# Kernel tuning notes

Hardware: AMD Instinct MI355X
Metric: run time of the kernel (lower is better)

## Reference

```python
import jax, jax.numpy as jnp
import numpy as np

HID = 256      # hard-coded hidden_size in the torch module
LEVELS = 16    # topological levels in the generated DAG


def _lstm_cell(x, h, c, Wih, Whh, bih, bhh):
    # PyTorch LSTM cell: gates ordered (input, forget, cell, output)
    g = x @ Wih.T + h @ Whh.T + bih + bhh
    i, f, gg, o = jnp.split(g, 4, axis=-1)
    c_new = jax.nn.sigmoid(f) * c + jax.nn.sigmoid(i) * jnp.tanh(gg)
    h_new = jax.nn.sigmoid(o) * jnp.tanh(c_new)
    return h_new, c_new


def _forward(tokens, parents_idx, parent_valid,
             Wih_tok, Whh_tok, bih_tok, bhh_tok,
             Wih_ins, Whh_ins, bih_ins, bhh_ins, Wlin, blin):
    N, T, E = tokens.shape
    K = N // LEVELS
    NEG = jnp.asarray(-1e30, tokens.dtype)

    # --- token-level LSTM over each instruction's tokens, batched across instrs ---
    def tok_step(carry, x):
        h, c = carry
        return _lstm_cell(x, h, c, Wih_tok, Whh_tok, bih_tok, bhh_tok), None
    z = jnp.zeros((N, HID), tokens.dtype)
    (ins_embed, _), _ = jax.lax.scan(tok_step, (z, z), tokens.transpose(1, 0, 2))
    # ins_embed: [N, HID] = final token-LSTM hidden per instruction

    # --- instruction-level LSTM over the DAG, level by level ---
    H = jnp.zeros((N, HID), tokens.dtype)
    C = jnp.zeros((N, HID), tokens.dtype)
    for l in range(LEVELS):
        sl = slice(l * K, (l + 1) * K)
        pidx = parents_idx[sl]                 # [K, P] indices into earlier levels
        pval = parent_valid[sl][..., None]     # [K, P, 1]
        ph = jnp.where(pval, H[pidx], NEG).max(axis=1)   # max-reduction combine
        pc = jnp.where(pval, C[pidx], NEG).max(axis=1)
        has = parent_valid[sl].any(axis=1, keepdims=True)
        h0 = jnp.where(has, ph, 0.0)           # no parents -> zero init_hidden
        c0 = jnp.where(has, pc, 0.0)
        h1, c1 = _lstm_cell(ins_embed[sl], h0, c0, Wih_ins, Whh_ins, bih_ins, bhh_ins)
        H = H.at[sl].set(h1)
        C = C.at[sl].set(c1)

    # roots = instructions with no children (never referenced as a parent)
    appears = jnp.zeros((N,), jnp.int32).at[parents_idx.reshape(-1)].add(
        parent_valid.reshape(-1).astype(jnp.int32))
    root = (appears == 0)[:, None]
    final = jnp.where(root, H, NEG).max(axis=0)   # [HID]
    return final @ Wlin.T + blin                   # [num_classes]


def setup_inputs() -> dict:
    N, T, E, P = 2048, 16, 512, 8
    K = N // LEVELS
    rng = np.random.default_rng(0)
    pidx = np.zeros((N, P), np.int32)
    pval = np.zeros((N, P), bool)
    for l in range(1, LEVELS):
        pidx[l * K:(l + 1) * K] = rng.integers(0, l * K, (K, P))
        pval[l * K:(l + 1) * K] = rng.random((K, P)) < 0.75
    key = jax.random.key(0)
    ks = jax.random.split(key, 6)
    s = lambda k, shape, fan: jax.random.normal(k, shape, jnp.float32) / np.float32(np.sqrt(fan))
    return {
        "tokens": jax.random.normal(ks[0], (N, T, E), jnp.float32),
        "parents_idx": jnp.asarray(pidx),
        "parent_valid": jnp.asarray(pval),
        "Wih_tok": s(ks[1], (4 * HID, E), E),
        "Whh_tok": s(ks[2], (4 * HID, HID), HID),
        "bih_tok": jnp.zeros((4 * HID,), jnp.float32),
        "bhh_tok": jnp.zeros((4 * HID,), jnp.float32),
        "Wih_ins": s(ks[3], (4 * HID, HID), HID),
        "Whh_ins": s(ks[4], (4 * HID, HID), HID),
        "bih_ins": jnp.zeros((4 * HID,), jnp.float32),
        "bhh_ins": jnp.zeros((4 * HID,), jnp.float32),
        "Wlin": s(ks[5], (1, HID), HID),
        "blin": jnp.zeros((1,), jnp.float32),
    }


def reference(tokens, parents_idx, parent_valid,
              Wih_tok, Whh_tok, bih_tok, bhh_tok,
              Wih_ins, Whh_ins, bih_ins, bhh_ins, Wlin, blin):
    return _forward(tokens, parents_idx, parent_valid,
                    Wih_tok, Whh_tok, bih_tok, bhh_tok,
                    Wih_ins, Whh_ins, bih_ins, bhh_ins, Wlin, blin)
```

## Files before the change

kernel.cpp:

```cpp
#include <hip/hip_runtime.h>

#define NTOK 2048
#define TT   16
#define EE   512
#define HIDD 256
#define G4   1024
#define NLVL 16
#define KLVL 128
#define INV2048 (1.0f/2048.0f)

typedef _Float16 v8h __attribute__((ext_vector_type(8)));
typedef _Float16 v4h __attribute__((ext_vector_type(4)));
typedef float    v4f __attribute__((ext_vector_type(4)));

__device__ __forceinline__ v4f mfma16(v8h a, v8h b, v4f c) {
  return __builtin_amdgcn_mfma_f32_16x16x32_f16(a, b, c, 0, 0, 0);
}

__device__ __forceinline__ float fsig(float x) {
  return 1.0f / (1.0f + __expf(-x));
}
__device__ __forceinline__ float ftanh(float x) {
  float ax = fabsf(x);
  float e  = __expf(-2.0f * ax);
  float t  = (1.0f - e) / (1.0f + e);
  return copysignf(t, x);
}

__device__ __forceinline__ void split8(const v4f& w0, const v4f& w1, v8h& hi, v8h& lo) {
#pragma unroll
  for (int u = 0; u < 4; ++u) {
    float v = w0[u]; _Float16 h = (_Float16)v;
    hi[u] = h; lo[u] = (_Float16)((v - (float)h) * 2048.0f);
  }
#pragma unroll
  for (int u = 0; u < 4; ++u) {
    float v = w1[u]; _Float16 h = (_Float16)v;
    hi[4+u] = h; lo[4+u] = (_Float16)((v - (float)h) * 2048.0f);
  }
}

__device__ __forceinline__ v8h cvt8(const v4f& w0, const v4f& w1) {
  v8h r;
#pragma unroll
  for (int u = 0; u < 4; ++u) { r[u] = (_Float16)w0[u]; r[4+u] = (_Float16)w1[u]; }
  return r;
}

__global__ __launch_bounds__(256) void knorm(const void* __restrict__ pv_raw,
                                             unsigned char* __restrict__ pv8) {
  __shared__ int mode;
  const int tid = threadIdx.x;
  if (tid == 0) mode = 0;
  __syncthreads();
  const unsigned* pu = (const unsigned*)pv_raw;
  int local = 0;
  for (int i = tid; i < 4096; i += 256) {
    unsigned v = pu[i];
    if (v == 0x3F800000u) { local = 2; break; }
    if (v > 1u) local = 1;
  }
  if (local) atomicMax(&mode, local);
  __syncthreads();
  const int m = mode;
  const unsigned char* pb = (const unsigned char*)pv_raw;
  const float* pf = (const float*)pv_raw;
  const int* pi = (const int*)pv_raw;
  for (int i = tid; i < NTOK * 8; i += 256) {
    unsigned char v;
    if (m == 1)      v = (pb[i] != 0);
    else if (m == 2) v = (pf[i] != 0.0f);
    else             v = (pi[i] != 0);
    pv8[i] = v;
  }
}

__global__ __launch_bounds__(256) void kw_cvt(
    const float* __restrict__ a0, _Float16* __restrict__ f0,
    const float* __restrict__ a1, _Float16* __restrict__ f1,
    const float* __restrict__ a2, _Float16* __restrict__ f2,
    const float* __restrict__ a3, _Float16* __restrict__ f3) {
  const int t = blockIdx.x * 256 + threadIdx.x;
  if (t < 32768) {
    const int row = t >> 5, col8 = (t & 31) * 8;
    const int fc = row >> 4, l15 = row & 15;
    const int kk = col8 >> 5, lq = (col8 >> 3) & 3;
    const int lane8 = (lq * 16 + l15) * 8;
    const size_t srow = (size_t)row * 256 + col8;
    {
      v4f x0 = *(const v4f*)(a0 + srow), x1 = *(const v4f*)(a0 + srow + 4);
      *(v8h*)(f0 + (size_t)(fc * 8 + kk) * 512 + lane8) = cvt8(x0, x1);
    }
    {
      v4f x0 = *(const v4f*)(a1 + srow), x1 = *(const v4f*)(a1 + srow + 4);
      v8h hi, lo; split8(x0, x1, hi, lo);
      _Float16* d = f1 + (size_t)(fc * 8 + kk) * 1024 + lane8;
      *(v8h*)d = hi; *(v8h*)(d + 512) = lo;
    }
    {
      v4f x0 = *(const v4f*)(a2 + srow), x1 = *(const v4f*)(a2 + srow + 4);
      v8h hi, lo; split8(x0, x1, hi, lo);
      _Float16* d = f2 + (size_t)(fc * 8 + kk) * 1024 + lane8;
      *(v8h*)d = hi; *(v8h*)(d + 512) = lo;
    }
  } else {
    const int k = t - 32768;
    const int row = k >> 6, col8 = (k & 63) * 8;
    const int fc = row >> 4, l15 = row & 15;
    const int kk = col8 >> 5, lq = (col8 >> 3) & 3;
    const size_t srow = (size_t)row * 512 + col8;
    v4f x0 = *(const v4f*)(a3 + srow), x1 = *(const v4f*)(a3 + srow + 4);
    *(v8h*)(f3 + (size_t)(fc * 16 + kk) * 512 + (lq * 16 + l15) * 8) = cvt8(x0, x1);
  }
}

__global__ __launch_bounds__(512, 1) void kg2(const float* __restrict__ A,
                                              const _Float16* __restrict__ WtH,
                                              const float* __restrict__ b1,
                                              const float* __restrict__ b2,
                                              _Float16* __restrict__ Xg, int h) {
  __shared__ _Float16 As[64 * 520];
  const int tid  = threadIdx.x;
  const int lane = tid & 63;
  const int nq   = tid >> 6;
  const int l15  = lane & 15;
  const int lq   = lane >> 4;
  const int m0   = blockIdx.x * 64;

#pragma unroll
  for (int p = 0; p < 4; ++p) {
    const int row  = p * 16 + (tid >> 5);
    const int col0 = (tid & 31) * 16;
    const int ar   = m0 + row;
    const int tokrow = (ar & 2047) * 16 + h * 8 + (ar >> 11);
    const float* s = A + (size_t)tokrow * EE + col0;
    v4f x0 = *(const v4f*)s, x1 = *(const v4f*)(s + 4);
    v4f x2 = *(const v4f*)(s + 8), x3 = *(const v4f*)(s + 12);
    _Float16* d = As + row * 520 + col0;
    *(v8h*)d       = cvt8(x0, x1);
    *(v8h*)(d + 8) = cvt8(x2, x3);
  }
  __syncthreads();

  v4f acc[4][8];
#pragma unroll
  for (int n = 0; n < 8; ++n) {
    const int col = (nq * 8 + n) * 16 + l15;
    const float bb = b1[col] + b2[col];
#pragma unroll
    for (int m = 0; m < 4; ++m) acc[m][n] = (v4f){bb, bb, bb, bb};
  }

#pragma unroll 4
  for (int kk = 0; kk < 16; ++kk) {
    v8h af[4];
#pragma unroll
    for (int m = 0; m < 4; ++m)
      af[m] = *(const v8h*)(As + (m * 16 + l15) * 520 + kk * 32 + lq * 8);
#pragma unroll
    for (int n = 0; n < 8; ++n) {
      const int fc = nq * 8 + n;
      v8h bh = *(const v8h*)(WtH + (size_t)(fc * 16 + kk) * 512 + lane * 8);
#pragma unroll
      for (int m = 0; m < 4; ++m) acc[m][n] = mfma16(af[m], bh, acc[m][n]);
    }
  }

#pragma unroll
  for (int m = 0; m < 4; ++m)
#pragma unroll
    for (int n = 0; n < 8; ++n) {
      const int row = m0 + m * 16 + lq * 4;
      const int col = (nq * 8 + n) * 16 + l15;
      v4h o;
#pragma unroll
      for (int r = 0; r < 4; ++r) o[r] = (_Float16)acc[m][n][r];
      *(v4h*)(Xg + ((size_t)(row >> 2) * G4 + col) * 4) = o;
    }
}

__global__ __launch_bounds__(512, 1) void kr3(const _Float16* __restrict__ Xg,
                                              const _Float16* __restrict__ WhhH,
                                              float* __restrict__ Hst,
                                              float* __restrict__ Cst,
                                              _Float16* __restrict__ emb, int q) {
  __shared__ float hbuf[2][16 * 260];
  const int tid  = threadIdx.x;
  const int lane = tid & 63;
  const int w    = tid >> 6;
  const int wv   = w & 3;
  const int jh   = w >> 2;
  const int l15  = lane & 15;
  const int lq   = lane >> 4;
  const int r0   = blockIdx.x * 16;

  const _Float16* wbase = WhhH + (size_t)(8 * jh + wv) * 4096 + lane * 8;

  v4f c[2];
  if (q) {
#pragma unroll
    for (int j2 = 0; j2 < 2; ++j2) {
      const int feat = 16 * (wv + 4 * (2 * jh + j2)) + l15;
#pragma unroll
      for (int r = 0; r < 4; ++r)
        c[j2][r] = Cst[(size_t)(r0 + lq * 4 + r) * HIDD + feat];
    }
    for (int idx = tid; idx < 4096; idx += 512)
      hbuf[0][(idx >> 8) * 260 + (idx & 255)] = Hst[(size_t)(r0 + (idx >> 8)) * HIDD + (idx & 255)];
  } else {
    c[0] = (v4f){0.f, 0.f, 0.f, 0.f};
    c[1] = (v4f){0.f, 0.f, 0.f, 0.f};
  }

  v4h xp[4][2];
  {
    const size_t xrow = (size_t)((r0 >> 2) + lq) * G4;
#pragma unroll
    for (int g = 0; g < 4; ++g)
#pragma unroll
      for (int j2 = 0; j2 < 2; ++j2) {
        const int col = 256 * g + 16 * (wv + 4 * (2 * jh + j2)) + l15;
        xp[g][j2] = *(const v4h*)(Xg + (xrow + col) * 4);
      }
  }

  v8h bA[8], bB[8];
#pragma unroll
  for (int g = 0; g < 4; ++g)
#pragma unroll
    for (int j2 = 0; j2 < 2; ++j2)
      bA[g * 2 + j2] = *(const v8h*)(wbase + (16 * g + 4 * j2) * 4096);
  __syncthreads();

#pragma unroll 1
  for (int tl = 0; tl < 8; ++tl) {
    const int cur = tl & 1;
    const bool have_h = (q > 0) || (tl > 0);
    v4f acc[4][2];
#pragma unroll
    for (int g = 0; g < 4; ++g)
#pragma unroll
      for (int j2 = 0; j2 < 2; ++j2) {
        v4f a;
#pragma unroll
        for (int r = 0; r < 4; ++r) a[r] = (float)xp[g][j2][r];
        acc[g][j2] = a;
      }
    if (tl < 7) {
      const size_t xrow = (size_t)((tl + 1) * 512 + (r0 >> 2) + lq) * G4;
#pragma unroll
      for (int g = 0; g < 4; ++g)
#pragma unroll
        for (int j2 = 0; j2 < 2; ++j2) {
          const int col = 256 * g + 16 * (wv + 4 * (2 * jh + j2)) + l15;
          xp[g][j2] = *(const v4h*)(Xg + (xrow + col) * 4);
        }
    }
    if (have_h) {
#pragma unroll
      for (int kp = 0; kp < 4; ++kp) {
        const int k0 = 2 * kp, k1 = 2 * kp + 1;
#pragma unroll
        for (int g = 0; g < 4; ++g)
#pragma unroll
          for (int j2 = 0; j2 < 2; ++j2)
            bB[g * 2 + j2] = *(const v8h*)(wbase + (16 * g + 4 * j2) * 4096 + k1 * 512);
        {
          const int ko = k0 * 32 + lq * 8;
          v4f w0 = *(const v4f*)(hbuf[cur] + l15 * 260 + ko);
          v4f w1 = *(const v4f*)(hbuf[cur] + l15 * 260 + ko + 4);
          v8h ah = cvt8(w0, w1);
#pragma unroll
          for (int g = 0; g < 4; ++g)
#pragma unroll
            for (int j2 = 0; j2 < 2; ++j2)
              acc[g][j2] = mfma16(ah, bA[g * 2 + j2], acc[g][j2]);
        }
        if (kp < 3) {
#pragma unroll
          for (int g = 0; g < 4; ++g)
#pragma unroll
            for (int j2 = 0; j2 < 2; ++j2)
              bA[g * 2 + j2] = *(const v8h*)(wbase + (16 * g + 4 * j2) * 4096 + (k1 + 1) * 512);
        }
        {
          const int ko = k1 * 32 + lq * 8;
          v4f w0 = *(const v4f*)(hbuf[cur] + l15 * 260 + ko);
          v4f w1 = *(const v4f*)(hbuf[cur] + l15 * 260 + ko + 4);
          v8h ah = cvt8(w0, w1);
#pragma unroll
          for (int g = 0; g < 4; ++g)
#pragma unroll
            for (int j2 = 0; j2 < 2; ++j2)
              acc[g][j2] = mfma16(ah, bB[g * 2 + j2], acc[g][j2]);
        }
      }
      if (tl < 7) {
#pragma unroll
        for (int g = 0; g < 4; ++g)
#pragma unroll
          for (int j2 = 0; j2 < 2; ++j2)
            bA[g * 2 + j2] = *(const v8h*)(wbase + (16 * g + 4 * j2) * 4096);
      }
    }
#pragma unroll
    for (int j2 = 0; j2 < 2; ++j2) {
      const int feat = 16 * (wv + 4 * (2 * jh + j2)) + l15;
#pragma unroll
      for (int r = 0; r < 4; ++r) {
        const int rr = lq * 4 + r;
        float cn = fsig(acc[1][j2][r]) * c[j2][r] + fsig(acc[0][j2][r]) * ftanh(acc[2][j2][r]);
        float hn = fsig(acc[3][j2][r]) * ftanh(cn);
        c[j2][r] = cn;
        hbuf[cur ^ 1][rr * 260 + feat] = hn;
        if (tl == 7) {
          const size_t grow = r0 + rr;
          if (!q) { Hst[grow * HIDD + feat] = hn; Cst[grow * HIDD + feat] = cn; }
          else    { emb[grow * HIDD + feat] = (_Float16)hn; }
        }
      }
    }
    __syncthreads();
  }
}

__global__ __launch_bounds__(512, 1) void kxi(const _Float16* __restrict__ emb,
                                              const _Float16* __restrict__ WihF,
                                              const float* __restrict__ bi,
                                              const float* __restrict__ bh,
                                              float* __restrict__ P) {
  __shared__ _Float16 As[64 * 264];
  const int tid  = threadIdx.x;
  const int lane = tid & 63;
  const int nq   = tid >> 6;
  const int l15  = lane & 15;
  const int lq   = lane >> 4;
  const int m0   = blockIdx.x * 64;

#pragma unroll
  for (int p = 0; p < 4; ++p) {
    const int idx = tid + 512 * p;
    const int row = idx >> 5;
    const int c8  = (idx & 31) * 8;
    *(v8h*)(As + row * 264 + c8) = *(const v8h*)(emb + (size_t)(m0 + row) * HIDD + c8);
  }
  __syncthreads();

  v4f acc[4][8];
#pragma unroll
  for (int n = 0; n < 8; ++n) {
    const int col = (nq * 8 + n) * 16 + l15;
    const float bb = bi[col] + bh[col];
#pragma unroll
    for (int m = 0; m < 4; ++m) acc[m][n] = (v4f){bb, bb, bb, bb};
  }

#pragma unroll 2
  for (int kk = 0; kk < 8; ++kk) {
    v8h af[4];
#pragma unroll
    for (int m = 0; m < 4; ++m)
      af[m] = *(const v8h*)(As + (m * 16 + l15) * 264 + kk * 32 + lq * 8);
#pragma unroll
    for (int n = 0; n < 8; ++n) {
      const int fc = nq * 8 + n;
      v8h bhf = *(const v8h*)(WihF + (size_t)(fc * 8 + kk) * 1024 + lane * 8);
#pragma unroll
      for (int m = 0; m < 4; ++m) acc[m][n] = mfma16(af[m], bhf, acc[m][n]);
    }
  }

#pragma unroll
  for (int m = 0; m < 4; ++m)
#pragma unroll
    for (int n = 0; n < 8; ++n) {
      const int row = m0 + m * 16 + lq * 4;
      const int col = (nq * 8 + n) * 16 + l15;
      *(v4f*)(P + ((size_t)(row >> 2) * G4 + col) * 4) = acc[m][n];
    }
}

__global__ __launch_bounds__(256) void kapp(const int* __restrict__ pidx,
                                            const unsigned char* __restrict__ pval,
                                            int* __restrict__ appears) {
  int e = blockIdx.x * 512 + threadIdx.x * 2;
#pragma unroll
  for (int u = 0; u < 2; ++u, ++e) {
    if (pval[e]) atomicAdd(appears + pidx[e], 1);
  }
}

__global__ __launch_bounds__(256) void klevel(
    const float* __restrict__ P,
    const _Float16* __restrict__ WhhF,
    const int* __restrict__ pidx, const unsigned char* __restrict__ pval,
    float* __restrict__ H, float* __restrict__ C, int l) {
  __shared__ _Float16 h0s[16 * 264];
  __shared__ float    c0s[16 * 68];
  __shared__ int      pis[128];
  __shared__ unsigned char pvs[128];
  const int tid  = threadIdx.x;
  const int lane = tid & 63;
  const int wv   = tid >> 6;
  const int l15  = lane & 15;
  const int lq   = lane >> 4;
  const int b    = blockIdx.x;
  const int mf   = b >> 2;
  const int q    = b & 3;
  const int fi   = q * 4 + wv;

  if (tid < 128) {
    int rr = tid >> 3, p = tid & 7;
    int row = l * KLVL + mf * 16 + rr;
    pis[tid] = pidx[row * 8 + p];
    pvs[tid] = pval[row * 8 + p];
  }
  __syncthreads();
#pragma unroll 1
  for (int it = 0; it < 4; ++it) {
    int task = tid + 256 * it;
    int rr = task >> 6;
    int f4 = (task & 63) * 4;
    v4f hm = (v4f){-1e30f, -1e30f, -1e30f, -1e30f};
    bool any = false;
#pragma unroll
    for (int p = 0; p < 8; ++p) {
      if (pvs[rr * 8 + p]) {
        any = true;
        v4f hv = *(const v4f*)(H + (size_t)pis[rr * 8 + p] * HIDD + f4);
#pragma unroll
        for (int u = 0; u < 4; ++u) hm[u] = fmaxf(hm[u], hv[u]);
      }
    }
    if (!any) hm = (v4f){0.f, 0.f, 0.f, 0.f};
    v4h h4;
#pragma unroll
    for (int u = 0; u < 4; ++u) h4[u] = (_Float16)hm[u];
    *(v4h*)(h0s + rr * 264 + f4) = h4;
  }
  {
    int rr = tid >> 4;
    int cc = (tid & 15) * 4;
    int f4 = q * 64 + cc;
    v4f cm = (v4f){-1e30f, -1e30f, -1e30f, -1e30f};
    bool any = false;
#pragma unroll
    for (int p = 0; p < 8; ++p) {
      if (pvs[rr * 8 + p]) {
        any = true;
        v4f cv = *(const v4f*)(C + (size_t)pis[rr * 8 + p] * HIDD + f4);
#pragma unroll
        for (int u = 0; u < 4; ++u) cm[u] = fmaxf(cm[u], cv[u]);
      }
    }
    if (!any) cm = (v4f){0.f, 0.f, 0.f, 0.f};
    *(v4f*)(c0s + rr * 68 + cc) = cm;
  }
  __syncthreads();

  v4f acc[4];
  const int lrow4 = l * 32 + mf * 4 + lq;
#pragma unroll
  for (int g = 0; g < 4; ++g)
    acc[g] = *(const v4f*)(P + ((size_t)lrow4 * G4 + 256 * g + 16 * fi + l15) * 4);

#pragma unroll 1
  for (int kk = 0; kk < 8; ++kk) {
    const int ko = kk * 32 + lq * 8;
    v8h ah = *(const v8h*)(h0s + l15 * 264 + ko);
#pragma unroll
    for (int g = 0; g < 4; ++g) {
      const int fc = 16 * g + fi;
      acc[g] = mfma16(ah, *(const v8h*)(WhhF + (size_t)(fc * 8 + kk) * 1024 + lane * 8), acc[g]);
    }
  }
#pragma unroll
  for (int r = 0; r < 4; ++r) {
    int rr = lq * 4 + r;
    int n  = 16 * fi + l15;
    float c0 = c0s[rr * 68 + 16 * wv + l15];
    float cn = fsig(acc[1][r]) * c0 + fsig(acc[0][r]) * ftanh(acc[2][r]);
    float hn = fsig(acc[3][r]) * ftanh(cn);
    int grow = l * KLVL + mf * 16 + rr;
    H[(size_t)grow * HIDD + n] = hn;
    C[(size_t)grow * HIDD + n] = cn;
  }
}

__global__ __launch_bounds__(256) void kroot1(const float* __restrict__ H,
                                              const int* __restrict__ appears,
                                              float* __restrict__ pmax) {
  __shared__ int app[64];
  const int tid = threadIdx.x;
  const int rb  = blockIdx.x * 64;
  if (tid < 64) app[tid] = appears[rb + tid];
  __syncthreads();
  float m = -1e30f;
#pragma unroll 1
  for (int r = 0; r < 64; ++r) {
    if (app[r] == 0) m = fmaxf(m, H[(size_t)(rb + r) * HIDD + tid]);
  }
  pmax[blockIdx.x * 256 + tid] = m;
}

__global__ __launch_bounds__(256) void kroot2(const float* __restrict__ pmax,
                                              const float* __restrict__ Wlin,
                                              const float* __restrict__ blin,
                                              float* __restrict__ out) {
  __shared__ float red[256];
  const int tid = threadIdx.x;
  float m = pmax[tid];
#pragma unroll 1
  for (int bb = 1; bb < 32; ++bb) m = fmaxf(m, pmax[bb * 256 + tid]);
  red[tid] = m * Wlin[tid];
  __syncthreads();
  if (tid == 0) {
    float s = 0.f;
    for (int i2 = 0; i2 < 256; ++i2) s += red[i2];
    out[0] = s + blin[0];
  }
}

extern "C" void kernel_launch(void* const* d_in, const int* in_sizes, int n_in,
                              void* d_out, int out_size, void* d_ws, size_t ws_size,
                              hipStream_t stream) {
  const float* tokens  = (const float*)d_in[0];
  const int*   pidx    = (const int*)d_in[1];
  const void*  pvraw   = (const void*)d_in[2];
  const float* Wih_tok = (const float*)d_in[3];
  const float* Whh_tok = (const float*)d_in[4];
  const float* bih_tok = (const float*)d_in[5];
  const float* bhh_tok = (const float*)d_in[6];
  const float* Wih_ins = (const float*)d_in[7];
  const float* Whh_ins = (const float*)d_in[8];
  const float* bih_ins = (const float*)d_in[9];
  const float* bhh_ins = (const float*)d_in[10];
  const float* Wlin    = (const float*)d_in[11];
  const float* blin    = (const float*)d_in[12];

  char* ws = (char*)d_ws;
  const size_t OFF_XG    = 0;
  const size_t OFF_H     = OFF_XG   + 33554432;
  const size_t OFF_C     = OFF_H    + 2097152;
  const size_t OFF_EMB   = OFF_C    + 2097152;
  const size_t OFF_P     = OFF_EMB  + 1048576;
  const size_t OFF_WHHT  = OFF_P    + 8388608;
  const size_t OFF_WIHIF = OFF_WHHT + 524288;
  const size_t OFF_WHHIF = OFF_WIHIF + 1048576;
  const size_t OFF_WTH   = OFF_WHHIF + 1048576;
  const size_t OFF_APP   = OFF_WTH  + 1048576;
  const size_t OFF_PMX   = OFF_APP  + 8192;
  const size_t OFF_PV8   = OFF_PMX  + 32768;

  _Float16* Xg    = (_Float16*)(ws + OFF_XG);
  float*    Hbuf  = (float*)(ws + OFF_H);
  float*    Cbuf  = (float*)(ws + OFF_C);
  _Float16* emb   = (_Float16*)(ws + OFF_EMB);
  float*    Pbuf  = (float*)(ws + OFF_P);
  _Float16* WhhT  = (_Float16*)(ws + OFF_WHHT);
  _Float16* WihIF = (_Float16*)(ws + OFF_WIHIF);
  _Float16* WhhIF = (_Float16*)(ws + OFF_WHHIF);
  _Float16* WtH   = (_Float16*)(ws + OFF_WTH);
  int*      app   = (int*)(ws + OFF_APP);
  float*    pmx   = (float*)(ws + OFF_PMX);
  unsigned char* pv8 = (unsigned char*)(ws + OFF_PV8);

  hipMemsetAsync(ws + OFF_APP, 0, 8192, stream);

  knorm<<<dim3(1), dim3(256), 0, stream>>>(pvraw, pv8);
  kw_cvt<<<dim3(384), dim3(256), 0, stream>>>(Whh_tok, WhhT,
                                              Wih_ins, WihIF,
                                              Whh_ins, WhhIF,
                                              Wih_tok, WtH);
  kapp<<<dim3(32), dim3(256), 0, stream>>>(pidx, pv8, app);

  for (int h = 0; h < 2; ++h) {
    kg2<<<dim3(256), dim3(512), 0, stream>>>(tokens, WtH, bih_tok, bhh_tok, Xg, h);
    kr3<<<dim3(128), dim3(512), 0, stream>>>(Xg, WhhT, Hbuf, Cbuf, emb, h);
  }

  kxi<<<dim3(32), dim3(512), 0, stream>>>(emb, WihIF, bih_ins, bhh_ins, Pbuf);

  for (int l = 0; l < NLVL; ++l) {
    klevel<<<dim3(32), dim3(256), 0, stream>>>(Pbuf, WhhIF, pidx, pv8,
                                               Hbuf, Cbuf, l);
  }
  kroot1<<<dim3(32), dim3(256), 0, stream>>>(Hbuf, app, pmx);
  kroot2<<<dim3(1), dim3(256), 0, stream>>>(pmx, Wlin, blin, (float*)d_out);
}
```

Baseline: 494.3 us.

## Stage recurrent Whh weight chunks through double-buffered LDS in token LSTM

The token-level recurrent kernel now has all threads cooperatively load each 32-wide K chunk of the fp16 Whh into a double-buffered shared-memory tile. Waves then read their MFMA B operands from LDS instead of each wave streaming its own slice from global memory into registers. The aim is more coalesced global loads, with the next chunk prefetched into registers while the current one is consumed. The cost is about 144 KB of LDS, an extra LDS write and read per weight element, and a block-wide barrier per K chunk. Weights are also fetched on the first step, when there is no hidden state to multiply.

New measurement: 660.1 us. +33.6%, slower.

```diff
diff --git a/kernel.cpp b/kernel.cpp
--- a/kernel.cpp
+++ b/kernel.cpp
@@ -179,12 +179,13 @@
     }
 }
 
-__global__ __launch_bounds__(512, 1) void kr3(const _Float16* __restrict__ Xg,
-                                              const _Float16* __restrict__ WhhH,
+__global__ __launch_bounds__(512, 1) void kr4(const _Float16* __restrict__ Xg,
+                                              const _Float16* __restrict__ WhhT,
                                               float* __restrict__ Hst,
                                               float* __restrict__ Cst,
                                               _Float16* __restrict__ emb, int q) {
-  __shared__ float hbuf[2][16 * 260];
+  __shared__ _Float16 wbuf[2][32768];
+  __shared__ float hbuf[16 * 260];
   const int tid  = threadIdx.x;
   const int lane = tid & 63;
   const int w    = tid >> 6;
@@ -194,8 +195,6 @@
   const int lq   = lane >> 4;
   const int r0   = blockIdx.x * 16;
 
-  const _Float16* wbase = WhhH + (size_t)(8 * jh + wv) * 4096 + lane * 8;
-
   v4f c[2];
   if (q) {
 #pragma unroll
@@ -206,7 +205,7 @@
         c[j2][r] = Cst[(size_t)(r0 + lq * 4 + r) * HIDD + feat];
     }
     for (int idx = tid; idx < 4096; idx += 512)
-      hbuf[0][(idx >> 8) * 260 + (idx & 255)] = Hst[(size_t)(r0 + (idx >> 8)) * HIDD + (idx & 255)];
+      hbuf[(idx >> 8) * 260 + (idx & 255)] = Hst[(size_t)(r0 + (idx >> 8)) * HIDD + (idx & 255)];
   } else {
     c[0] = (v4f){0.f, 0.f, 0.f, 0.f};
     c[1] = (v4f){0.f, 0.f, 0.f, 0.f};
@@ -224,17 +223,16 @@
       }
   }
 
-  v8h bA[8], bB[8];
-#pragma unroll
-  for (int g = 0; g < 4; ++g)
-#pragma unroll
-    for (int j2 = 0; j2 < 2; ++j2)
-      bA[g * 2 + j2] = *(const v8h*)(wbase + (16 * g + 4 * j2) * 4096);
+  v8h rS[8];
+#pragma unroll
+  for (int i = 0; i < 8; ++i) {
+    const int ch = tid + 512 * i;
+    rS[i] = *(const v8h*)(WhhT + (size_t)((ch >> 6) * 8 + 0) * 512 + (ch & 63) * 8);
+  }
   __syncthreads();
 
 #pragma unroll 1
   for (int tl = 0; tl < 8; ++tl) {
-    const int cur = tl & 1;
     const bool have_h = (q > 0) || (tl > 0);
     v4f acc[4][2];
 #pragma unroll
@@ -256,53 +254,39 @@
           xp[g][j2] = *(const v4h*)(Xg + (xrow + col) * 4);
         }
     }
-    if (have_h) {
-#pragma unroll
-      for (int kp = 0; kp < 4; ++kp) {
-        const int k0 = 2 * kp, k1 = 2 * kp + 1;
+
+#pragma unroll
+    for (int s = 0; s < 8; ++s) {
+      _Float16* wb = wbuf[s & 1];
+#pragma unroll
+      for (int i = 0; i < 8; ++i)
+        *(v8h*)(wb + (tid + 512 * i) * 8) = rS[i];
+      {
+        const int kkn = (s + 1) & 7;
+#pragma unroll
+        for (int i = 0; i < 8; ++i) {
+          const int ch = tid + 512 * i;
+          rS[i] = *(const v8h*)(WhhT + (size_t)((ch >> 6) * 8 + kkn) * 512 + (ch & 63) * 8);
+        }
+      }
+      __syncthreads();
+      if (have_h) {
+        const int ko = s * 32 + lq * 8;
+        v4f w0 = *(const v4f*)(hbuf + l15 * 260 + ko);
+        v4f w1 = *(const v4f*)(hbuf + l15 * 260 + ko + 4);
+        v8h ah = cvt8(w0, w1);
 #pragma unroll
         for (int g = 0; g < 4; ++g)
 #pragma unroll
-          for (int j2 = 0; j2 < 2; ++j2)
-            bB[g * 2 + j2] = *(const v8h*)(wbase + (16 * g + 4 * j2) * 4096 + k1 * 512);
-        {
-          const int ko = k0 * 32 + lq * 8;
-          v4f w0 = *(const v4f*)(hbuf[cur] + l15 * 260 + ko);
-          v4f w1 = *(const v4f*)(hbuf[cur] + l15 * 260 + ko + 4);
-          v8h ah = cvt8(w0, w1);
-#pragma unroll
-          for (int g = 0; g < 4; ++g)
-#pragma unroll
-            for (int j2 = 0; j2 < 2; ++j2)
-              acc[g][j2] = mfma16(ah, bA[g * 2 + j2], acc[g][j2]);
-        }
-        if (kp < 3) {
-#pragma unroll
-          for (int g = 0; g < 4; ++g)
-#pragma unroll
-            for (int j2 = 0; j2 < 2; ++j2)
-              bA[g * 2 + j2] = *(const v8h*)(wbase + (16 * g + 4 * j2) * 4096 + (k1 + 1) * 512);
-        }
-        {
-          const int ko = k1 * 32 + lq * 8;
-          v4f w0 = *(const v4f*)(hbuf[cur] + l15 * 260 + ko);
-          v4f w1 = *(const v4f*)(hbuf[cur] + l15 * 260 + ko + 4);
-          v8h ah = cvt8(w0, w1);
-#pragma unroll
-          for (int g = 0; g < 4; ++g)
-#pragma unroll
-            for (int j2 = 0; j2 < 2; ++j2)
-              acc[g][j2] = mfma16(ah, bB[g * 2 + j2], acc[g][j2]);
-        }
-      }
-      if (tl < 7) {
-#pragma unroll
-        for (int g = 0; g < 4; ++g)
-#pragma unroll
-          for (int j2 = 0; j2 < 2; ++j2)
-            bA[g * 2 + j2] = *(const v8h*)(wbase + (16 * g + 4 * j2) * 4096);
-      }
-    }
+          for (int j2 = 0; j2 < 2; ++j2) {
+            const int fc = 16 * g + 8 * jh + 4 * j2 + wv;
+            v8h b = *(const v8h*)(wb + fc * 512 + lane * 8);
+            acc[g][j2] = mfma16(ah, b, acc[g][j2]);
+          }
+      }
+    }
+    __syncthreads();
+
 #pragma unroll
     for (int j2 = 0; j2 < 2; ++j2) {
       const int feat = 16 * (wv + 4 * (2 * jh + j2)) + l15;
@@ -312,7 +296,7 @@
         float cn = fsig(acc[1][j2][r]) * c[j2][r] + fsig(acc[0][j2][r]) * ftanh(acc[2][j2][r]);
         float hn = fsig(acc[3][j2][r]) * ftanh(cn);
         c[j2][r] = cn;
-        hbuf[cur ^ 1][rr * 260 + feat] = hn;
+        hbuf[rr * 260 + feat] = hn;
         if (tl == 7) {
           const size_t grow = r0 + rr;
           if (!q) { Hst[grow * HIDD + feat] = hn; Cst[grow * HIDD + feat] = cn; }
@@ -320,7 +304,6 @@
         }
       }
     }
-    __syncthreads();
   }
 }
 
@@ -576,7 +559,7 @@
 
   for (int h = 0; h < 2; ++h) {
     kg2<<<dim3(256), dim3(512), 0, stream>>>(tokens, WtH, bih_tok, bhh_tok, Xg, h);
-    kr3<<<dim3(128), dim3(512), 0, stream>>>(Xg, WhhT, Hbuf, Cbuf, emb, h);
+    kr4<<<dim3(128), dim3(512), 0, stream>>>(Xg, WhhT, Hbuf, Cbuf, emb, h);
   }
 
   kxi<<<dim3(32), dim3(512), 0, stream>>>(emb, WihIF, bih_ins, bhh_ins, Pbuf);
```
